# Optimization experiments

Hardware: AMD Instinct MI355X
Metric: run time of the kernel (lower is better)

Reference implementation:

```python
import jax, jax.numpy as jnp
import numpy as np

D_MODEL, N_HEADS, N_KV, THETA = 2048, 16, 4, 10000.0
HEAD_DIM = D_MODEL // N_HEADS  # 128


def _rope_sin_cos(seq_len, head_dim, theta):
    inv_freq = 1.0 / theta ** (jnp.arange(0, head_dim, 2, dtype=jnp.float32) / head_dim)
    pos = jnp.arange(seq_len, dtype=jnp.float32)
    freqs = pos[:, None] * inv_freq[None, :]              # [S, hd/2]
    emb = jnp.concatenate([freqs, freqs], axis=-1)        # [S, hd]
    return jnp.sin(emb), jnp.cos(emb)


def _rotate_half(t):
    h = t.shape[-1] // 2
    return jnp.concatenate([-t[..., h:], t[..., :h]], axis=-1)


def _apply_rope(t, sin, cos):
    # t: [B, H, S, hd]; sin/cos: [S, hd]
    return t * cos[None, None] + _rotate_half(t) * sin[None, None]


def setup_inputs() -> dict:
    key = jax.random.key(0)
    ks = jax.random.split(key, 5)
    B, S = 4, 2048
    scale = 1.0 / np.sqrt(D_MODEL)
    return {
        "x": jax.random.normal(ks[0], (B, S, D_MODEL), jnp.float32),
        "Wq": jax.random.normal(ks[1], (D_MODEL, N_HEADS * HEAD_DIM), jnp.float32) * scale,
        "Wk": jax.random.normal(ks[2], (D_MODEL, N_KV * HEAD_DIM), jnp.float32) * scale,
        "Wv": jax.random.normal(ks[3], (D_MODEL, N_KV * HEAD_DIM), jnp.float32) * scale,
        "Wo": jax.random.normal(ks[4], (N_HEADS * HEAD_DIM, D_MODEL), jnp.float32) * scale,
    }


def reference(x, Wq, Wk, Wv, Wo):
    B, S, _ = x.shape
    G = N_HEADS // N_KV  # query heads per kv head

    q = (x @ Wq).reshape(B, S, N_HEADS, HEAD_DIM).transpose(0, 2, 1, 3)  # [B,H,S,hd]
    k = (x @ Wk).reshape(B, S, N_KV, HEAD_DIM).transpose(0, 2, 1, 3)     # [B,KV,S,hd]
    v = (x @ Wv).reshape(B, S, N_KV, HEAD_DIM).transpose(0, 2, 1, 3)

    sin, cos = _rope_sin_cos(S, HEAD_DIM, THETA)
    q = _apply_rope(q, sin, cos)
    k = _apply_rope(k, sin, cos)

    # grouped attention: avoid materializing repeated kv heads
    qg = q.reshape(B, N_KV, G, S, HEAD_DIM)
    scores = jnp.einsum("bkgqd,bksd->bkgqs", qg, k) / np.sqrt(HEAD_DIM)
    causal = jnp.tril(jnp.ones((S, S), dtype=bool))
    scores = jnp.where(causal[None, None, None], scores, jnp.finfo(scores.dtype).min)
    attn = jax.nn.softmax(scores, axis=-1)
    out = jnp.einsum("bkgqs,bksd->bkgqd", attn, v)          # [B,KV,G,S,hd]
    out = out.reshape(B, N_HEADS, S, HEAD_DIM).transpose(0, 2, 1, 3).reshape(B, S, N_HEADS * HEAD_DIM)
    return out @ Wo
```

## Files before the change

kernel.cpp:

```cpp
#include <hip/hip_runtime.h>
#include <hip/hip_bf16.h>

#define DMODEL 2048
#define NHEADS 16
#define NKV 4
#define HD 128
#define SEQ 2048
#define BATCH 4

typedef __attribute__((ext_vector_type(2))) float f32x2;
typedef __attribute__((ext_vector_type(4))) float f32x4;
typedef __attribute__((ext_vector_type(16))) float f32x16;
typedef __attribute__((ext_vector_type(8))) short bf16x8;
typedef __attribute__((ext_vector_type(4))) unsigned int u32x4;

static __device__ __forceinline__ float bf2f(short u) {
    unsigned int x = ((unsigned int)(unsigned short)u) << 16;
    return __builtin_bit_cast(float, x);
}
static __device__ __forceinline__ short f2bf(float f) {
    unsigned int x = __builtin_bit_cast(unsigned int, f);
    unsigned int r = (x + 0x7fffu + ((x >> 16) & 1u)) >> 16;
    return (short)r;
}
static __device__ __forceinline__ unsigned int cvtpk_bf16(float lo, float hi) {
    unsigned int r;
    asm("v_cvt_pk_bf16_f32 %0, %1, %2" : "=v"(r) : "v"(lo), "v"(hi));
    return r;
}
static __device__ __forceinline__ float fexp2(float x) {
    float r;
    asm("v_exp_f32 %0, %1" : "=v"(r) : "v"(x));
    return r;
}
static __device__ __forceinline__ float ffract(float x) {
    float r;
    asm("v_fract_f32 %0, %1" : "=v"(r) : "v"(x));
    return r;
}
static __device__ __forceinline__ float fsin01(float x) {
    float r;
    asm("v_sin_f32 %0, %1" : "=v"(r) : "v"(x));
    return r;
}
static __device__ __forceinline__ float fcos01(float x) {
    float r;
    asm("v_cos_f32 %0, %1" : "=v"(r) : "v"(x));
    return r;
}
static __device__ __forceinline__ void gload16(const void* g, void* l) {
    __builtin_amdgcn_global_load_lds((const __attribute__((address_space(1))) void*)g,
                                     (__attribute__((address_space(3))) void*)l, 16, 0, 0);
}
static __device__ __forceinline__ void wbar6() {
    asm volatile("s_waitcnt vmcnt(6)" ::: "memory");
    __builtin_amdgcn_s_barrier();
    asm volatile("" ::: "memory");
}
static __device__ __forceinline__ void wbar4() {
    asm volatile("s_waitcnt vmcnt(4)" ::: "memory");
    __builtin_amdgcn_s_barrier();
    asm volatile("" ::: "memory");
}
static __device__ __forceinline__ void wbar6lg() {
    asm volatile("s_waitcnt vmcnt(6) lgkmcnt(0)" ::: "memory");
    __builtin_amdgcn_s_barrier();
    asm volatile("" ::: "memory");
}
static __device__ __forceinline__ void wbar0lg() {
    asm volatile("s_waitcnt vmcnt(0) lgkmcnt(0)" ::: "memory");
    __builtin_amdgcn_s_barrier();
    asm volatile("" ::: "memory");
}
static __device__ __forceinline__ void bar() {
    __builtin_amdgcn_s_barrier();
    asm volatile("" ::: "memory");
}

__global__ __launch_bounds__(256)
void prep(const float* __restrict__ x, short* __restrict__ xb,
          const float* __restrict__ Wq, const float* __restrict__ Wk,
          const float* __restrict__ Wv, const float* __restrict__ Wo,
          short* __restrict__ WqkvT, short* __restrict__ WoT) {
    __shared__ short Ts[64 * 72];
    const int bid = blockIdx.x, tid = threadIdx.x;

    if (bid < 2048) {
        const int n8 = BATCH * SEQ * DMODEL / 8;
        for (int i = bid * 256 + tid; i < n8; i += 2048 * 256) {
            float4 a = ((const float4*)x)[(size_t)i * 2];
            float4 b = ((const float4*)x)[(size_t)i * 2 + 1];
            bf16x8 o;
            o[0] = f2bf(a.x); o[1] = f2bf(a.y); o[2] = f2bf(a.z); o[3] = f2bf(a.w);
            o[4] = f2bf(b.x); o[5] = f2bf(b.y); o[6] = f2bf(b.z); o[7] = f2bf(b.w);
            ((bf16x8*)xb)[i] = o;
        }
        return;
    }

    const float* W;
    short* Wt;
    int C, r0, c0;
    if (bid < 3072) {
        int id = bid - 2048;
        W = Wq; Wt = WqkvT; C = 2048;
        c0 = (id & 31) * 64; r0 = (id >> 5) * 64;
    } else if (bid < 3328) {
        int id = bid - 3072;
        W = Wk; Wt = WqkvT + (size_t)2048 * 2048; C = 512;
        c0 = (id & 7) * 64; r0 = (id >> 3) * 64;
    } else if (bid < 3584) {
        int id = bid - 3328;
        W = Wv; Wt = WqkvT + (size_t)2560 * 2048; C = 512;
        c0 = (id & 7) * 64; r0 = (id >> 3) * 64;
    } else {
        int id = bid - 3584;
        W = Wo; Wt = WoT; C = 2048;
        c0 = (id & 31) * 64; r0 = (id >> 5) * 64;
    }
    const int R = 2048;
    for (int it = 0; it < 4; ++it) {
        int idx = it * 256 + tid;
        int row = idx >> 4, col4 = (idx & 15) * 4;
        float4 t = *(const float4*)&W[(size_t)(r0 + row) * C + c0 + col4];
        Ts[(col4 + 0) * 72 + row] = f2bf(t.x);
        Ts[(col4 + 1) * 72 + row] = f2bf(t.y);
        Ts[(col4 + 2) * 72 + row] = f2bf(t.z);
        Ts[(col4 + 3) * 72 + row] = f2bf(t.w);
    }
    __syncthreads();
    for (int it = 0; it < 2; ++it) {
        int idx = it * 256 + tid;
        int n = idx >> 3, k8 = (idx & 7) * 8;
        bf16x8 o = *(const bf16x8*)&Ts[n * 72 + k8];
        *(bf16x8*)&Wt[(size_t)(c0 + n) * R + r0 + k8] = o;
    }
}

template <int MODE>
__global__ __launch_bounds__(256, 2)
void gemm_sb(const short* __restrict__ A, const short* __restrict__ B,
             void* __restrict__ Cp, int M, int N, int K, int nbx) {
    __shared__ short As[256 * 64];
    __shared__ short Bs[128 * 64];
    const int tid = threadIdx.x, lane = tid & 63, w = tid >> 6;
    const int wr = w >> 1, wc = w & 1, lr = lane & 15, lg = lane >> 4;

    const int nwg = gridDim.x;
    const int qq = nwg >> 3, rr = nwg & 7;
    const int xcd = blockIdx.x & 7, loc = blockIdx.x >> 3;
    const int wg = (xcd < rr ? xcd * (qq + 1) : rr * (qq + 1) + (xcd - rr) * qq) + loc;
    const int m0 = (wg / nbx) * 256, n0 = (wg % nbx) * 128;

    const int srcchunk = ((lane & 7) ^ (lane >> 3)) * 8;
    const int lrow = w * 8;
    const int grow = w * 8 + (lane >> 3);

#define STG_A(T, HA)                                                              \
    {                                                                             \
        _Pragma("unroll") for (int i = 0; i < 4; ++i)                             \
            gload16(&A[(size_t)(m0 + (HA) * 128 + i * 32 + grow) * K +            \
                       (size_t)(T) * 64 + srcchunk],                              \
                    &As[((HA) * 128 + i * 32 + lrow) * 64]);                      \
    }
#define STG_B(T, HB)                                                              \
    {                                                                             \
        _Pragma("unroll") for (int i = 0; i < 2; ++i)                             \
            gload16(&B[(size_t)(n0 + (HB) * 64 + i * 32 + grow) * K +             \
                       (size_t)(T) * 64 + srcchunk],                              \
                    &Bs[((HB) * 64 + i * 32 + lrow) * 64]);                       \
    }

    f32x4 acc[2][4][2][2] = {};
    const int NT = K >> 6;

    STG_A(0, 0);
    STG_B(0, 0);
    STG_B(0, 1);
    STG_A(0, 1);

    bf16x8 af0[4][2], af1[4][2], bf0[2][2], bf1[2][2];
    for (int kt = 0; kt < NT; ++kt) {
        const int Tn = (kt + 1 < NT) ? kt + 1 : kt;

        wbar6();
#pragma unroll
        for (int q = 0; q < 4; ++q)
#pragma unroll
            for (int kk = 0; kk < 2; ++kk)
                af0[q][kk] = *(const bf16x8*)&As[(wr * 64 + q * 16 + lr) * 64 +
                                                 (((kk * 4 + lg) ^ (lr & 7)) << 3)];
#pragma unroll
        for (int r = 0; r < 2; ++r)
#pragma unroll
            for (int kk = 0; kk < 2; ++kk)
                bf0[r][kk] = *(const bf16x8*)&Bs[(wc * 32 + r * 16 + lr) * 64 +
                                                 (((kk * 4 + lg) ^ (lr & 7)) << 3)];
        __builtin_amdgcn_s_setprio(1);
#pragma unroll
        for (int q = 0; q < 4; ++q)
#pragma unroll
            for (int r = 0; r < 2; ++r)
#pragma unroll
                for (int kk = 0; kk < 2; ++kk)
                    acc[0][q][0][r] = __builtin_amdgcn_mfma_f32_16x16x32_bf16(
                        af0[q][kk], bf0[r][kk], acc[0][q][0][r], 0, 0, 0);
        __builtin_amdgcn_s_setprio(0);

        wbar4();
#pragma unroll
        for (int r = 0; r < 2; ++r)
#pragma unroll
            for (int kk = 0; kk < 2; ++kk)
                bf1[r][kk] = *(const bf16x8*)&Bs[(64 + wc * 32 + r * 16 + lr) * 64 +
                                                 (((kk * 4 + lg) ^ (lr & 7)) << 3)];
        STG_A(Tn, 0);
        STG_B(Tn, 0);
        __builtin_amdgcn_s_setprio(1);
#pragma unroll
        for (int q = 0; q < 4; ++q)
#pragma unroll
            for (int r = 0; r < 2; ++r)
#pragma unroll
                for (int kk = 0; kk < 2; ++kk)
                    acc[0][q][1][r] = __builtin_amdgcn_mfma_f32_16x16x32_bf16(
                        af0[q][kk], bf1[r][kk], acc[0][q][1][r], 0, 0, 0);
        __builtin_amdgcn_s_setprio(0);

        wbar6();
#pragma unroll
        for (int q = 0; q < 4; ++q)
#pragma unroll
            for (int kk = 0; kk < 2; ++kk)
                af1[q][kk] = *(const bf16x8*)&As[(128 + wr * 64 + q * 16 + lr) * 64 +
                                                 (((kk * 4 + lg) ^ (lr & 7)) << 3)];
        STG_B(Tn, 1);
        __builtin_amdgcn_s_setprio(1);
#pragma unroll
        for (int q = 0; q < 4; ++q)
#pragma unroll
            for (int r = 0; r < 2; ++r)
#pragma unroll
                for (int kk = 0; kk < 2; ++kk)
                    acc[1][q][0][r] = __builtin_amdgcn_mfma_f32_16x16x32_bf16(
                        af1[q][kk], bf0[r][kk], acc[1][q][0][r], 0, 0, 0);
        __builtin_amdgcn_s_setprio(0);

        bar();
        STG_A(Tn, 1);
        __builtin_amdgcn_s_setprio(1);
#pragma unroll
        for (int q = 0; q < 4; ++q)
#pragma unroll
            for (int r = 0; r < 2; ++r)
#pragma unroll
                for (int kk = 0; kk < 2; ++kk)
                    acc[1][q][1][r] = __builtin_amdgcn_mfma_f32_16x16x32_bf16(
                        af1[q][kk], bf1[r][kk], acc[1][q][1][r], 0, 0, 0);
        __builtin_amdgcn_s_setprio(0);
    }
    asm volatile("s_waitcnt vmcnt(0)" ::: "memory");

    if (MODE == 2 && n0 < 2560) {
        short* Cb = (short*)Cp;
        const float scl = (n0 >= 2048) ? 0.12751744695179782f : 1.0f;
        const float c13 = 13.287712379549449f / 64.0f;
        const float inv2pi = 0.15915494309189535f;
        float invf2[2];
#pragma unroll
        for (int r = 0; r < 2; ++r)
            invf2[r] = fexp2(-(float)(wc * 32 + r * 16 + lr) * c13) * inv2pi;
#pragma unroll
        for (int hA = 0; hA < 2; ++hA)
#pragma unroll
            for (int q = 0; q < 4; ++q)
#pragma unroll
                for (int r = 0; r < 2; ++r)
#pragma unroll
                    for (int j = 0; j < 4; ++j) {
                        int row = m0 + hA * 128 + wr * 64 + q * 16 + lg * 4 + j;
                        int pos = row & (SEQ - 1);
                        float fr = ffract((float)pos * invf2[r]);
                        float s = fsin01(fr), c = fcos01(fr);
                        float v0 = acc[hA][q][0][r][j];
                        float v1 = acc[hA][q][1][r][j];
                        int col0 = n0 + wc * 32 + r * 16 + lr;
                        Cb[(size_t)row * N + col0] = f2bf((v0 * c - v1 * s) * scl);
                        Cb[(size_t)row * N + col0 + 64] = f2bf((v1 * c + v0 * s) * scl);
                    }
    } else {
#pragma unroll
        for (int hA = 0; hA < 2; ++hA)
#pragma unroll
            for (int q = 0; q < 4; ++q)
#pragma unroll
                for (int hB = 0; hB < 2; ++hB)
#pragma unroll
                    for (int r = 0; r < 2; ++r)
#pragma unroll
                        for (int j = 0; j < 4; ++j) {
                            int row = m0 + hA * 128 + wr * 64 + q * 16 + lg * 4 + j;
                            int col = n0 + hB * 64 + wc * 32 + r * 16 + lr;
                            float v = acc[hA][q][hB][r][j];
                            if (MODE == 1) ((float*)Cp)[(size_t)row * N + col] = v;
                            else ((short*)Cp)[(size_t)row * N + col] = f2bf(v);
                        }
    }
#undef STG_A
#undef STG_B
}

template <bool A_F32, bool C_F32>
__global__ __launch_bounds__(256)
void gemm_kernel(const void* __restrict__ Ap, const float* __restrict__ Bp,
                 void* __restrict__ Cp, int M, int N, int K) {
    const int BK = 32, PAD = 8, LDT = BK + PAD;
    __shared__ short As[128 * LDT];
    __shared__ short Bt[128 * LDT];
    const int tid = threadIdx.x;
    const int lane = tid & 63, w = tid >> 6;
    const int wr = w >> 1, wc = w & 1;
    const int lr = lane & 15, lg = lane >> 4;
    const int m0 = blockIdx.y * 128, n0 = blockIdx.x * 128;
    f32x4 acc[4][4] = {};

    for (int k0 = 0; k0 < K; k0 += BK) {
        __syncthreads();
        for (int it = 0; it < 4; ++it) {
            int row = (tid >> 3) + it * 32;
            int kk = (tid & 7) * 4;
            short4 o;
            if (A_F32) {
                const float* A = (const float*)Ap;
                float4 t = *(const float4*)&A[(size_t)(m0 + row) * K + k0 + kk];
                o.x = f2bf(t.x); o.y = f2bf(t.y); o.z = f2bf(t.z); o.w = f2bf(t.w);
            } else {
                const short* A = (const short*)Ap;
                o = *(const short4*)&A[(size_t)(m0 + row) * K + k0 + kk];
            }
            *(short4*)&As[row * LDT + kk] = o;
        }
        for (int it = 0; it < 4; ++it) {
            int krow = (tid >> 5) + it * 8;
            int col = (tid & 31) * 4;
            float4 t = *(const float4*)&Bp[(size_t)(k0 + krow) * N + n0 + col];
            Bt[(col + 0) * LDT + krow] = f2bf(t.x);
            Bt[(col + 1) * LDT + krow] = f2bf(t.y);
            Bt[(col + 2) * LDT + krow] = f2bf(t.z);
            Bt[(col + 3) * LDT + krow] = f2bf(t.w);
        }
        __syncthreads();
        bf16x8 af[4], bfr[4];
        for (int rb = 0; rb < 4; ++rb)
            af[rb] = *(const bf16x8*)&As[(wr * 64 + rb * 16 + lr) * LDT + lg * 8];
        for (int cb = 0; cb < 4; ++cb)
            bfr[cb] = *(const bf16x8*)&Bt[(wc * 64 + cb * 16 + lr) * LDT + lg * 8];
        for (int rb = 0; rb < 4; ++rb)
            for (int cb = 0; cb < 4; ++cb)
                acc[rb][cb] = __builtin_amdgcn_mfma_f32_16x16x32_bf16(
                    af[rb], bfr[cb], acc[rb][cb], 0, 0, 0);
    }

    for (int rb = 0; rb < 4; ++rb)
        for (int cb = 0; cb < 4; ++cb)
            for (int j = 0; j < 4; ++j) {
                int row = m0 + wr * 64 + rb * 16 + lg * 4 + j;
                int col = n0 + wc * 64 + cb * 16 + lr;
                float v = acc[rb][cb][j];
                if (C_F32) ((float*)Cp)[(size_t)row * N + col] = v;
                else ((short*)Cp)[(size_t)row * N + col] = f2bf(v);
            }
}

__global__ __launch_bounds__(256)
void rope_kernel(short* __restrict__ Qp, int ldq, short* __restrict__ Kp, int ldk) {
    const int QP = BATCH * SEQ * NHEADS * 64;
    const int KP = BATCH * SEQ * NKV * 64;
    const int total = QP + KP;
    const float kscale = 0.12751744695179782f;
    for (int idx = blockIdx.x * blockDim.x + threadIdx.x; idx < total;
         idx += gridDim.x * blockDim.x) {
        short* base;
        size_t off;
        int i, row;
        float scl;
        if (idx < QP) {
            i = idx & 63;
            int hh = (idx >> 6) & (NHEADS - 1);
            row = idx >> 10;
            base = Qp;
            off = (size_t)row * ldq + hh * HD;
            scl = 1.0f;
        } else {
            int t = idx - QP;
            i = t & 63;
            int hh = (t >> 6) & (NKV - 1);
            row = t >> 8;
            base = Kp;
            off = (size_t)row * ldk + hh * HD;
            scl = kscale;
        }
        int pos = row & (SEQ - 1);
        float invf = exp2f(-(float)i * (13.287712379549449f / 64.0f));
        float ang = (float)pos * invf;
        float s, c;
        sincosf(ang, &s, &c);
        float t1 = bf2f(base[off + i]);
        float t2 = bf2f(base[off + i + 64]);
        base[off + i] = f2bf((t1 * c - t2 * s) * scl);
        base[off + i + 64] = f2bf((t2 * c + t1 * s) * scl);
    }
}

__global__ __launch_bounds__(512, 2)
void attn_kernel(const short* __restrict__ Qp, int ldq,
                 const short* __restrict__ Kp, int ldk,
                 const short* __restrict__ Vp, int ldv,
                 short* __restrict__ O) {
    __shared__ short Ks[3][64 * 128];
    __shared__ short Vt[2][128 * 64];

    const int tid = threadIdx.x, lane = tid & 63, w = tid >> 6;
    const int l31 = lane & 31, lh = lane >> 5, l7 = lane & 7;
    const int hq = blockIdx.y, b = blockIdx.z;
    const int kvh = hq >> 2;
    const size_t brow = (size_t)b * SEQ;

    const int d0 = (tid & 15) * 8;
    const int rvb = (tid >> 4) * 2;
    bf16x8 vreg[2];

#define STAGE_K(T, BUF)                                                              \
    {                                                                                \
        _Pragma("unroll") for (int it = 0; it < 2; ++it) {                           \
            int row = w * 8 + it * 4 + (lane >> 4);                                  \
            int cblk = (lane & 15) ^ (row & 7);                                      \
            gload16(&Kp[(brow + (size_t)(T) * 64 + row) * ldk + kvh * HD + cblk * 8],\
                    &Ks[BUF][(w * 8 + it * 4) * 128]);                               \
        }                                                                            \
    }
#define LOAD_V(T)                                                                    \
    {                                                                                \
        _Pragma("unroll") for (int h2 = 0; h2 < 2; ++h2)                             \
            vreg[h2] = *(const bf16x8*)&Vp[(brow + (size_t)(T) * 64 + rvb + h2) *    \
                                           ldv + kvh * HD + d0];                     \
    }
#define WRITE_V(BUF)                                                                 \
    {                                                                                \
        _Pragma("unroll") for (int e = 0; e < 8; ++e) {                              \
            int dd = d0 + e;                                                         \
            int gg = (e ^ (tid & 15)) & 7;                                           \
            unsigned int pk = ((unsigned int)(unsigned short)vreg[0][e]) |           \
                              (((unsigned int)(unsigned short)vreg[1][e]) << 16);    \
            *(unsigned int*)&Vt[BUF][dd * 64 + (((rvb >> 3) ^ gg) << 3) + (rvb & 7)] = pk;\
        }                                                                            \
    }

    for (int pass = 0; pass < 2; ++pass) {
        const int qt = (pass == 0) ? (int)blockIdx.x : 7 - (int)blockIdx.x;
        const int q0 = qt * 256;
        const int qrow = q0 + w * 32 + l31;

        bf16x8 qf[8];
#pragma unroll
        for (int kc = 0; kc < 8; ++kc)
            qf[kc] = *(const bf16x8*)&Qp[(brow + qrow) * ldq + hq * HD +
                                         kc * 16 + lh * 8];

        f32x16 oacc[4] = {};
        float mrun = -__builtin_inff(), lrun = 0.f;

        const int ntiles = 4 * qt + 4;

        __syncthreads();
        STAGE_K(0, 0);
        LOAD_V(0);
        __syncthreads();
        WRITE_V(0);
        STAGE_K(1, 1);
        LOAD_V(1);
        __syncthreads();

        int cur = 0;
        int kcur = 0;
        for (int t = 0; t < ntiles; ++t) {
            const int nxt = cur ^ 1;
            const bool pre = (t + 1 < ntiles);
            const bool deep = (t + 2 < ntiles);
            const int kb2 = (kcur >= 1) ? kcur - 1 : kcur + 2;

            if (deep) { STAGE_K(t + 2, kb2); }

            f32x16 sacc[2] = {};
            __builtin_amdgcn_s_setprio(1);
#pragma unroll
            for (int kvb = 0; kvb < 2; ++kvb) {
                const int kvrow = kvb * 32 + l31;
#pragma unroll
                for (int kc = 0; kc < 8; ++kc) {
                    int c = kc * 2 + lh;
                    int cp = (c & 8) | ((c ^ l7) & 7);
                    bf16x8 kf = *(const bf16x8*)&Ks[kcur][kvrow * 128 + cp * 8];
                    sacc[kvb] = __builtin_amdgcn_mfma_f32_32x32x16_bf16(
                        kf, qf[kc], sacc[kvb], 0, 0, 0);
                }
            }
            __builtin_amdgcn_s_setprio(0);

            const int kv0 = t * 64;
            float st[32];
            const bool need_mask = (kv0 + 63 > qrow);
#pragma unroll
            for (int kvb = 0; kvb < 2; ++kvb)
#pragma unroll
                for (int r = 0; r < 16; ++r) {
                    float s = sacc[kvb][r];
                    if (need_mask) {
                        int kvloc = kvb * 32 + (r & 3) + 8 * (r >> 2) + 4 * lh;
                        if (kv0 + kvloc > qrow) s = -__builtin_inff();
                    }
                    st[kvb * 16 + r] = s;
                }

            f32x2 p2[16];
#pragma unroll
            for (int i = 0; i < 16; ++i) p2[i] = (f32x2){st[2 * i], st[2 * i + 1]};

            f32x2 x8[8], x4[4], x2v[2], x1;
#pragma unroll
            for (int i = 0; i < 8; ++i) x8[i] = __builtin_elementwise_max(p2[i], p2[i + 8]);
#pragma unroll
            for (int i = 0; i < 4; ++i) x4[i] = __builtin_elementwise_max(x8[i], x8[i + 4]);
            x2v[0] = __builtin_elementwise_max(x4[0], x4[2]);
            x2v[1] = __builtin_elementwise_max(x4[1], x4[3]);
            x1 = __builtin_elementwise_max(x2v[0], x2v[1]);
            float rowmax = fmaxf(x1[0], x1[1]);
            rowmax = fmaxf(rowmax, __shfl_xor(rowmax, 32, 64));

            if (!__all(rowmax <= mrun + 11.54f)) {
                float mnew = fmaxf(mrun, rowmax);
                float alpha = fexp2(mrun - mnew);
                lrun *= alpha;
#pragma unroll
                for (int db = 0; db < 4; ++db)
#pragma unroll
                    for (int r = 0; r < 16; ++r) oacc[db][r] *= alpha;
                mrun = mnew;
            }
            const f32x2 mr2 = (f32x2){mrun, mrun};
#pragma unroll
            for (int i = 0; i < 16; ++i) {
                f32x2 d = p2[i] - mr2;
                st[2 * i] = fexp2(d[0]);
                st[2 * i + 1] = fexp2(d[1]);
            }
            f32x2 q2[16];
#pragma unroll
            for (int i = 0; i < 16; ++i) q2[i] = (f32x2){st[2 * i], st[2 * i + 1]};
            f32x2 t8[8], t4[4], t2v[2], t1;
#pragma unroll
            for (int i = 0; i < 8; ++i) t8[i] = q2[i] + q2[i + 8];
#pragma unroll
            for (int i = 0; i < 4; ++i) t4[i] = t8[i] + t8[i + 4];
            t2v[0] = t4[0] + t4[2];
            t2v[1] = t4[1] + t4[3];
            t1 = t2v[0] + t2v[1];
            float rs = t1[0] + t1[1];
            rs += __shfl_xor(rs, 32, 64);
            lrun += rs;

            if (pre) {
                WRITE_V(nxt);
                if (deep) { LOAD_V(t + 2); }
            }

            u32x4 pfrag[4];
#pragma unroll
            for (int kvc = 0; kvc < 4; ++kvc) {
                int base2 = (kvc >> 1) * 16 + (kvc & 1) * 8;
                unsigned int lo0 = cvtpk_bf16(st[base2 + 0], st[base2 + 1]);
                unsigned int lo1 = cvtpk_bf16(st[base2 + 2], st[base2 + 3]);
                unsigned int hi0 = cvtpk_bf16(st[base2 + 4], st[base2 + 5]);
                unsigned int hi1 = cvtpk_bf16(st[base2 + 6], st[base2 + 7]);
                unsigned int rlo0 = __shfl_xor(lo0, 32, 64);
                unsigned int rlo1 = __shfl_xor(lo1, 32, 64);
                unsigned int rhi0 = __shfl_xor(hi0, 32, 64);
                unsigned int rhi1 = __shfl_xor(hi1, 32, 64);
                u32x4 pu;
                pu[0] = lh ? rhi0 : lo0;
                pu[1] = lh ? rhi1 : lo1;
                pu[2] = lh ? hi0 : rlo0;
                pu[3] = lh ? hi1 : rlo1;
                pfrag[kvc] = pu;
            }

            __builtin_amdgcn_s_setprio(1);
#pragma unroll
            for (int db = 0; db < 4; ++db) {
                const int d = db * 32 + l31;
                const int g = (d ^ (d >> 3)) & 7;
#pragma unroll
                for (int kvc = 0; kvc < 4; ++kvc) {
                    int cp = ((kvc * 2 + lh) ^ g) & 7;
                    bf16x8 vf = *(const bf16x8*)&Vt[cur][d * 64 + cp * 8];
                    oacc[db] = __builtin_amdgcn_mfma_f32_32x32x16_bf16(
                        vf, __builtin_bit_cast(bf16x8, pfrag[kvc]), oacc[db], 0, 0, 0);
                }
            }
            __builtin_amdgcn_s_setprio(0);

            if (pre) {
                if (deep) { wbar6lg(); } else { wbar0lg(); }
                cur = nxt;
                kcur = (kcur < 2) ? kcur + 1 : 0;
            }
        }

        const float invl = 1.0f / lrun;
#pragma unroll
        for (int db = 0; db < 4; ++db)
#pragma unroll
            for (int j = 0; j < 4; ++j) {
                short4 o4;
                o4.x = f2bf(oacc[db][j * 4 + 0] * invl);
                o4.y = f2bf(oacc[db][j * 4 + 1] * invl);
                o4.z = f2bf(oacc[db][j * 4 + 2] * invl);
                o4.w = f2bf(oacc[db][j * 4 + 3] * invl);
                *(short4*)&O[(brow + qrow) * DMODEL + hq * HD +
                             db * 32 + 8 * j + 4 * lh] = o4;
            }
    }
#undef STAGE_K
#undef LOAD_V
#undef WRITE_V
}

extern "C" void kernel_launch(void* const* d_in, const int* in_sizes, int n_in,
                              void* d_out, int out_size, void* d_ws, size_t ws_size,
                              hipStream_t stream) {
    const float* x = (const float*)d_in[0];
    const float* Wq = (const float*)d_in[1];
    const float* Wk = (const float*)d_in[2];
    const float* Wv = (const float*)d_in[3];
    const float* Wo = (const float*)d_in[4];
    float* out = (float*)d_out;

    const size_t BS = (size_t)BATCH * SEQ;
    dim3 blk(256);

    const size_t planA_shorts = BS * 2048 + BS * 3072 + (size_t)3072 * 2048 + (size_t)2048 * 2048;
    if (ws_size >= planA_shorts * 2) {
        short* xb = (short*)d_ws;
        short* QKV = xb + BS * 2048;
        short* WqkvT = QKV + BS * 3072;
        short* WoT = WqkvT + (size_t)3072 * 2048;
        short* AO = xb;

        prep<<<dim3(4608), blk, 0, stream>>>(x, xb, Wq, Wk, Wv, Wo, WqkvT, WoT);
        gemm_sb<2><<<dim3(768), blk, 0, stream>>>(xb, WqkvT, (void*)QKV,
                                                  8192, 3072, 2048, 24);
        attn_kernel<<<dim3(4, NHEADS, BATCH), dim3(512), 0, stream>>>(
            QKV, 3072, QKV + 2048, 3072, QKV + 2560, 3072, AO);
        gemm_sb<1><<<dim3(512), blk, 0, stream>>>(AO, WoT, (void*)out,
                                                  8192, 2048, 2048, 16);
    } else {
        short* Qb = (short*)d_ws;
        short* Kb = Qb + BS * DMODEL;
        short* Vb = Kb + BS * (NKV * HD);
        short* AO = Vb + BS * (NKV * HD);
        gemm_kernel<true, false><<<dim3(16, 64), blk, 0, stream>>>((const void*)x, Wq, (void*)Qb, 8192, 2048, 2048);
        gemm_kernel<true, false><<<dim3(4, 64), blk, 0, stream>>>((const void*)x, Wk, (void*)Kb, 8192, 512, 2048);
        gemm_kernel<true, false><<<dim3(4, 64), blk, 0, stream>>>((const void*)x, Wv, (void*)Vb, 8192, 512, 2048);
        rope_kernel<<<dim3(4096), blk, 0, stream>>>(Qb, 2048, Kb, 512);
        attn_kernel<<<dim3(4, NHEADS, BATCH), dim3(512), 0, stream>>>(
            Qb, 2048, Kb, 512, Vb, 512, AO);
        gemm_kernel<false, true><<<dim3(16, 64), blk, 0, stream>>>((const void*)AO, Wo, (void*)out, 8192, 2048, 2048);
    }
}
```

Before: 322.0 us.

## Software-pipeline QK^T of next tile with softmax of current tile

The attention loop is unrolled by two with ping-pong score accumulators, so the QK^T MFMAs for tile t+1 are issued before the softmax and PV of tile t. The goal is to overlap matrix-core work with the exponent and reduction VALU work. The barrier wait count drops from vmcnt(6) to vmcnt(2), so the K tile staged two steps ahead is resident one iteration earlier. The extra 32 accumulator registers raise register pressure, and the tighter wait can expose more global-load latency.

New measurement: 408.3 us. 1.27x slower.

```diff
diff --git a/kernel.cpp b/kernel.cpp
--- a/kernel.cpp
+++ b/kernel.cpp
@@ -62,8 +62,8 @@
     __builtin_amdgcn_s_barrier();
     asm volatile("" ::: "memory");
 }
-static __device__ __forceinline__ void wbar6lg() {
-    asm volatile("s_waitcnt vmcnt(6) lgkmcnt(0)" ::: "memory");
+static __device__ __forceinline__ void wbar2lg() {
+    asm volatile("s_waitcnt vmcnt(2) lgkmcnt(0)" ::: "memory");
     __builtin_amdgcn_s_barrier();
     asm volatile("" ::: "memory");
 }
@@ -455,6 +455,123 @@
             *(unsigned int*)&Vt[BUF][dd * 64 + (((rvb >> 3) ^ gg) << 3) + (rvb & 7)] = pk;\
         }                                                                            \
     }
+#define QK_ISSUE(SDST, KBUF)                                                         \
+    {                                                                                \
+        SDST[0] = (f32x16){};                                                        \
+        SDST[1] = (f32x16){};                                                        \
+        __builtin_amdgcn_s_setprio(1);                                               \
+        _Pragma("unroll") for (int kvb = 0; kvb < 2; ++kvb) {                        \
+            const int kvrow = kvb * 32 + l31;                                        \
+            _Pragma("unroll") for (int kc = 0; kc < 8; ++kc) {                       \
+                int c = kc * 2 + lh;                                                 \
+                int cp = (c & 8) | ((c ^ l7) & 7);                                   \
+                bf16x8 kf = *(const bf16x8*)&Ks[KBUF][kvrow * 128 + cp * 8];         \
+                SDST[kvb] = __builtin_amdgcn_mfma_f32_32x32x16_bf16(                 \
+                    kf, qf[kc], SDST[kvb], 0, 0, 0);                                 \
+            }                                                                        \
+        }                                                                            \
+        __builtin_amdgcn_s_setprio(0);                                               \
+    }
+#define TILE_BODY(T, SCUR, SNEXT)                                                    \
+    {                                                                                \
+        const int nxt = cur ^ 1;                                                     \
+        const bool pre = ((T) + 1 < ntiles);                                         \
+        const bool deep = ((T) + 2 < ntiles);                                        \
+        const int kb2 = (kcur >= 1) ? kcur - 1 : kcur + 2;                           \
+        const int knx = (kcur < 2) ? kcur + 1 : 0;                                   \
+        if (deep) { STAGE_K((T) + 2, kb2); }                                         \
+        if (pre) { QK_ISSUE(SNEXT, knx); }                                           \
+        const int kv0 = (T) * 64;                                                    \
+        float st[32];                                                                \
+        const bool need_mask = (kv0 + 63 > qrow);                                    \
+        _Pragma("unroll") for (int kvb = 0; kvb < 2; ++kvb)                          \
+            _Pragma("unroll") for (int r = 0; r < 16; ++r) {                         \
+                float s = SCUR[kvb][r];                                              \
+                if (need_mask) {                                                     \
+                    int kvloc = kvb * 32 + (r & 3) + 8 * (r >> 2) + 4 * lh;          \
+                    if (kv0 + kvloc > qrow) s = -__builtin_inff();                   \
+                }                                                                    \
+                st[kvb * 16 + r] = s;                                                \
+            }                                                                        \
+        f32x2 p2[16];                                                                \
+        _Pragma("unroll") for (int i = 0; i < 16; ++i)                               \
+            p2[i] = (f32x2){st[2 * i], st[2 * i + 1]};                               \
+        f32x2 x8[8], x4[4], x2v[2], x1;                                              \
+        _Pragma("unroll") for (int i = 0; i < 8; ++i)                                \
+            x8[i] = __builtin_elementwise_max(p2[i], p2[i + 8]);                     \
+        _Pragma("unroll") for (int i = 0; i < 4; ++i)                                \
+            x4[i] = __builtin_elementwise_max(x8[i], x8[i + 4]);                     \
+        x2v[0] = __builtin_elementwise_max(x4[0], x4[2]);                            \
+        x2v[1] = __builtin_elementwise_max(x4[1], x4[3]);                            \
+        x1 = __builtin_elementwise_max(x2v[0], x2v[1]);                              \
+        float rowmax = fmaxf(x1[0], x1[1]);                                          \
+        rowmax = fmaxf(rowmax, __shfl_xor(rowmax, 32, 64));                          \
+        if (!__all(rowmax <= mrun + 11.54f)) {                                       \
+            float mnew = fmaxf(mrun, rowmax);                                        \
+            float alpha = fexp2(mrun - mnew);                                        \
+            lrun *= alpha;                                                           \
+            _Pragma("unroll") for (int db = 0; db < 4; ++db)                         \
+                _Pragma("unroll") for (int r = 0; r < 16; ++r) oacc[db][r] *= alpha; \
+            mrun = mnew;                                                             \
+        }                                                                            \
+        const f32x2 mr2 = (f32x2){mrun, mrun};                                       \
+        _Pragma("unroll") for (int i = 0; i < 16; ++i) {                             \
+            f32x2 dd2 = p2[i] - mr2;                                                 \
+            st[2 * i] = fexp2(dd2[0]);                                               \
+            st[2 * i + 1] = fexp2(dd2[1]);                                           \
+        }                                                                            \
+        f32x2 q2[16];                                                                \
+        _Pragma("unroll") for (int i = 0; i < 16; ++i)                               \
+            q2[i] = (f32x2){st[2 * i], st[2 * i + 1]};                               \
+        f32x2 t8[8], t4[4], t2v[2], t1;                                              \
+        _Pragma("unroll") for (int i = 0; i < 8; ++i) t8[i] = q2[i] + q2[i + 8];     \
+        _Pragma("unroll") for (int i = 0; i < 4; ++i) t4[i] = t8[i] + t8[i + 4];     \
+        t2v[0] = t4[0] + t4[2];                                                      \
+        t2v[1] = t4[1] + t4[3];                                                      \
+        t1 = t2v[0] + t2v[1];                                                        \
+        float rs = t1[0] + t1[1];                                                    \
+        rs += __shfl_xor(rs, 32, 64);                                                \
+        lrun += rs;                                                                  \
+        if (pre) {                                                                   \
+            WRITE_V(nxt);                                                            \
+            if (deep) { LOAD_V((T) + 2); }                                           \
+        }                                                                            \
+        u32x4 pfrag[4];                                                              \
+        _Pragma("unroll") for (int kvc = 0; kvc < 4; ++kvc) {                        \
+            int base2 = (kvc >> 1) * 16 + (kvc & 1) * 8;                             \
+            unsigned int lo0 = cvtpk_bf16(st[base2 + 0], st[base2 + 1]);             \
+            unsigned int lo1 = cvtpk_bf16(st[base2 + 2], st[base2 + 3]);             \
+            unsigned int hi0 = cvtpk_bf16(st[base2 + 4], st[base2 + 5]);             \
+            unsigned int hi1 = cvtpk_bf16(st[base2 + 6], st[base2 + 7]);             \
+            unsigned int rlo0 = __shfl_xor(lo0, 32, 64);                             \
+            unsigned int rlo1 = __shfl_xor(lo1, 32, 64);                             \
+            unsigned int rhi0 = __shfl_xor(hi0, 32, 64);                             \
+            unsigned int rhi1 = __shfl_xor(hi1, 32, 64);                             \
+            u32x4 pu;                                                                \
+            pu[0] = lh ? rhi0 : lo0;                                                 \
+            pu[1] = lh ? rhi1 : lo1;                                                 \
+            pu[2] = lh ? hi0 : rlo0;                                                 \
+            pu[3] = lh ? hi1 : rlo1;                                                 \
+            pfrag[kvc] = pu;                                                         \
+        }                                                                            \
+        __builtin_amdgcn_s_setprio(1);                                               \
+        _Pragma("unroll") for (int db = 0; db < 4; ++db) {                           \
+            const int d = db * 32 + l31;                                             \
+            const int g = (d ^ (d >> 3)) & 7;                                        \
+            _Pragma("unroll") for (int kvc = 0; kvc < 4; ++kvc) {                    \
+                int cp = ((kvc * 2 + lh) ^ g) & 7;                                   \
+                bf16x8 vf = *(const bf16x8*)&Vt[cur][d * 64 + cp * 8];               \
+                oacc[db] = __builtin_amdgcn_mfma_f32_32x32x16_bf16(                  \
+                    vf, __builtin_bit_cast(bf16x8, pfrag[kvc]), oacc[db], 0, 0, 0);  \
+            }                                                                        \
+        }                                                                            \
+        __builtin_amdgcn_s_setprio(0);                                               \
+        if (pre) {                                                                   \
+            if (deep) { wbar2lg(); } else { wbar0lg(); }                             \
+            cur = nxt;                                                               \
+            kcur = knx;                                                              \
+        }                                                                            \
+    }
 
     for (int pass = 0; pass < 2; ++pass) {
         const int qt = (pass == 0) ? (int)blockIdx.x : 7 - (int)blockIdx.x;
@@ -483,137 +600,12 @@
 
         int cur = 0;
         int kcur = 0;
-        for (int t = 0; t < ntiles; ++t) {
-            const int nxt = cur ^ 1;
-            const bool pre = (t + 1 < ntiles);
-            const bool deep = (t + 2 < ntiles);
-            const int kb2 = (kcur >= 1) ? kcur - 1 : kcur + 2;
-
-            if (deep) { STAGE_K(t + 2, kb2); }
-
-            f32x16 sacc[2] = {};
-            __builtin_amdgcn_s_setprio(1);
-#pragma unroll
-            for (int kvb = 0; kvb < 2; ++kvb) {
-                const int kvrow = kvb * 32 + l31;
-#pragma unroll
-                for (int kc = 0; kc < 8; ++kc) {
-                    int c = kc * 2 + lh;
-                    int cp = (c & 8) | ((c ^ l7) & 7);
-                    bf16x8 kf = *(const bf16x8*)&Ks[kcur][kvrow * 128 + cp * 8];
-                    sacc[kvb] = __builtin_amdgcn_mfma_f32_32x32x16_bf16(
-                        kf, qf[kc], sacc[kvb], 0, 0, 0);
-                }
-            }
-            __builtin_amdgcn_s_setprio(0);
-
-            const int kv0 = t * 64;
-            float st[32];
-            const bool need_mask = (kv0 + 63 > qrow);
-#pragma unroll
-            for (int kvb = 0; kvb < 2; ++kvb)
-#pragma unroll
-                for (int r = 0; r < 16; ++r) {
-                    float s = sacc[kvb][r];
-                    if (need_mask) {
-                        int kvloc = kvb * 32 + (r & 3) + 8 * (r >> 2) + 4 * lh;
-                        if (kv0 + kvloc > qrow) s = -__builtin_inff();
-                    }
-                    st[kvb * 16 + r] = s;
-                }
-
-            f32x2 p2[16];
-#pragma unroll
-            for (int i = 0; i < 16; ++i) p2[i] = (f32x2){st[2 * i], st[2 * i + 1]};
-
-            f32x2 x8[8], x4[4], x2v[2], x1;
-#pragma unroll
-            for (int i = 0; i < 8; ++i) x8[i] = __builtin_elementwise_max(p2[i], p2[i + 8]);
-#pragma unroll
-            for (int i = 0; i < 4; ++i) x4[i] = __builtin_elementwise_max(x8[i], x8[i + 4]);
-            x2v[0] = __builtin_elementwise_max(x4[0], x4[2]);
-            x2v[1] = __builtin_elementwise_max(x4[1], x4[3]);
-            x1 = __builtin_elementwise_max(x2v[0], x2v[1]);
-            float rowmax = fmaxf(x1[0], x1[1]);
-            rowmax = fmaxf(rowmax, __shfl_xor(rowmax, 32, 64));
-
-            if (!__all(rowmax <= mrun + 11.54f)) {
-                float mnew = fmaxf(mrun, rowmax);
-                float alpha = fexp2(mrun - mnew);
-                lrun *= alpha;
-#pragma unroll
-                for (int db = 0; db < 4; ++db)
-#pragma unroll
-                    for (int r = 0; r < 16; ++r) oacc[db][r] *= alpha;
-                mrun = mnew;
-            }
-            const f32x2 mr2 = (f32x2){mrun, mrun};
-#pragma unroll
-            for (int i = 0; i < 16; ++i) {
-                f32x2 d = p2[i] - mr2;
-                st[2 * i] = fexp2(d[0]);
-                st[2 * i + 1] = fexp2(d[1]);
-            }
-            f32x2 q2[16];
-#pragma unroll
-            for (int i = 0; i < 16; ++i) q2[i] = (f32x2){st[2 * i], st[2 * i + 1]};
-            f32x2 t8[8], t4[4], t2v[2], t1;
-#pragma unroll
-            for (int i = 0; i < 8; ++i) t8[i] = q2[i] + q2[i + 8];
-#pragma unroll
-            for (int i = 0; i < 4; ++i) t4[i] = t8[i] + t8[i + 4];
-            t2v[0] = t4[0] + t4[2];
-            t2v[1] = t4[1] + t4[3];
-            t1 = t2v[0] + t2v[1];
-            float rs = t1[0] + t1[1];
-            rs += __shfl_xor(rs, 32, 64);
-            lrun += rs;
-
-            if (pre) {
-                WRITE_V(nxt);
-                if (deep) { LOAD_V(t + 2); }
-            }
-
-            u32x4 pfrag[4];
-#pragma unroll
-            for (int kvc = 0; kvc < 4; ++kvc) {
-                int base2 = (kvc >> 1) * 16 + (kvc & 1) * 8;
-                unsigned int lo0 = cvtpk_bf16(st[base2 + 0], st[base2 + 1]);
-                unsigned int lo1 = cvtpk_bf16(st[base2 + 2], st[base2 + 3]);
-                unsigned int hi0 = cvtpk_bf16(st[base2 + 4], st[base2 + 5]);
-                unsigned int hi1 = cvtpk_bf16(st[base2 + 6], st[base2 + 7]);
-                unsigned int rlo0 = __shfl_xor(lo0, 32, 64);
-                unsigned int rlo1 = __shfl_xor(lo1, 32, 64);
-                unsigned int rhi0 = __shfl_xor(hi0, 32, 64);
-                unsigned int rhi1 = __shfl_xor(hi1, 32, 64);
-                u32x4 pu;
-                pu[0] = lh ? rhi0 : lo0;
-                pu[1] = lh ? rhi1 : lo1;
-                pu[2] = lh ? hi0 : rlo0;
-                pu[3] = lh ? hi1 : rlo1;
-                pfrag[kvc] = pu;
-            }
-
-            __builtin_amdgcn_s_setprio(1);
-#pragma unroll
-            for (int db = 0; db < 4; ++db) {
-                const int d = db * 32 + l31;
-                const int g = (d ^ (d >> 3)) & 7;
-#pragma unroll
-                for (int kvc = 0; kvc < 4; ++kvc) {
-                    int cp = ((kvc * 2 + lh) ^ g) & 7;
-                    bf16x8 vf = *(const bf16x8*)&Vt[cur][d * 64 + cp * 8];
-                    oacc[db] = __builtin_amdgcn_mfma_f32_32x32x16_bf16(
-                        vf, __builtin_bit_cast(bf16x8, pfrag[kvc]), oacc[db], 0, 0, 0);
-                }
-            }
-            __builtin_amdgcn_s_setprio(0);
-
-            if (pre) {
-                if (deep) { wbar6lg(); } else { wbar0lg(); }
-                cur = nxt;
-                kcur = (kcur < 2) ? kcur + 1 : 0;
-            }
+        f32x16 sA[2], sB[2];
+        QK_ISSUE(sA, 0);
+
+        for (int t = 0; t < ntiles; t += 2) {
+            TILE_BODY(t, sA, sB);
+            TILE_BODY(t + 1, sB, sA);
         }
 
         const float invl = 1.0f / lrun;
@@ -633,6 +625,8 @@
 #undef STAGE_K
 #undef LOAD_V
 #undef WRITE_V
+#undef QK_ISSUE
+#undef TILE_BODY
 }
 
 extern "C" void kernel_launch(void* const* d_in, const int* in_sizes, int n_in,
```

## Add 256x256-tile 8-wave pipelined GEMM for output projection

Applied to the files above, without the earlier changes.

Adds a new bf16 MFMA GEMM kernel with 256x256 tiles, 512 threads, double-buffered swizzled LDS, and interleaved staging of the next K tiles between MFMA quarter-steps with setprio. It also remaps block IDs across the 8 XCDs for locality. It replaces the 128-tile gemm_sb for the Wo projection, aiming for more data reuse per tile and better overlap of loads with compute. The trade-off is higher LDS and register use, which limits occupancy, and a grid of only 256 blocks.

After: 324.0 us. About the same (+0.6%).

```diff
diff --git a/kernel.cpp b/kernel.cpp
--- a/kernel.cpp
+++ b/kernel.cpp
@@ -308,6 +308,155 @@
     }
 #undef STG_A
 #undef STG_B
+}
+
+__global__ __launch_bounds__(512, 2)
+void gemm8(const short* __restrict__ A, const short* __restrict__ B,
+           float* __restrict__ C, int M, int N, int K, int nbx) {
+    __shared__ short As[2][256 * 64];
+    __shared__ short Bs[2][256 * 64];
+    const int tid = threadIdx.x, lane = tid & 63, w = tid >> 6;
+    const int wm = w >> 2, wn = w & 3;
+    const int lr = lane & 15, lg = lane >> 4;
+    const int l8 = lane >> 3, l7 = lane & 7;
+
+    const int nwg = gridDim.x;
+    const int qq = nwg >> 3, rr = nwg & 7;
+    const int xcd = blockIdx.x & 7, loc = blockIdx.x >> 3;
+    const int wg = (xcd < rr ? xcd * (qq + 1) : rr * (qq + 1) + (xcd - rr) * qq) + loc;
+    const int m0 = (wg / nbx) * 256, n0 = (wg % nbx) * 256;
+
+    const int srcchunk = (l7 ^ l8) * 8;
+    const int NT = K >> 6;
+
+#define STG_A8(T, MH, BUF)                                                         \
+    {                                                                              \
+        _Pragma("unroll") for (int j = 0; j < 2; ++j)                              \
+            gload16(&A[(size_t)(m0 + j * 128 + (MH) * 64 + w * 8 + l8) * K +       \
+                       (size_t)(T) * 64 + srcchunk],                               \
+                    &As[BUF][(j * 128 + (MH) * 64 + w * 8) * 64]);                 \
+    }
+#define STG_B8(T, NH, BUF)                                                         \
+    {                                                                              \
+        _Pragma("unroll") for (int j = 0; j < 2; ++j) {                            \
+            int rbase = (j * 2 + (w >> 2)) * 64 + (NH) * 32 + (w & 3) * 8;         \
+            gload16(&B[(size_t)(n0 + rbase + l8) * K +                             \
+                       (size_t)(T) * 64 + srcchunk],                               \
+                    &Bs[BUF][rbase * 64]);                                         \
+        }                                                                          \
+    }
+
+    f32x4 acc[2][4][2][2] = {};
+
+    STG_A8(0, 0, 0);
+    STG_A8(0, 1, 0);
+    STG_B8(0, 0, 0);
+    STG_B8(0, 1, 0);
+    STG_A8(1, 0, 1);
+    STG_B8(1, 0, 1);
+    wbar4();
+
+    bf16x8 af[4][2], b0[2][2], b1[2][2];
+    for (int t = 0; t < NT; ++t) {
+        const int bt = t & 1;
+        const int tn1 = (t + 1 < NT) ? t + 1 : NT - 1;
+        const int tn2 = (t + 2 < NT) ? t + 2 : NT - 1;
+        const int bn1 = tn1 & 1, bn2 = tn2 & 1;
+
+#pragma unroll
+        for (int mf = 0; mf < 4; ++mf)
+#pragma unroll
+            for (int kk = 0; kk < 2; ++kk)
+                af[mf][kk] = *(const bf16x8*)&As[bt][(wm * 128 + mf * 16 + lr) * 64 +
+                                                    (((kk * 4 + lg) ^ (lr & 7)) << 3)];
+#pragma unroll
+        for (int nf = 0; nf < 2; ++nf)
+#pragma unroll
+            for (int kk = 0; kk < 2; ++kk)
+                b0[nf][kk] = *(const bf16x8*)&Bs[bt][(wn * 64 + nf * 16 + lr) * 64 +
+                                                     (((kk * 4 + lg) ^ (lr & 7)) << 3)];
+        STG_A8(tn1, 1, bn1);
+        __builtin_amdgcn_s_setprio(1);
+#pragma unroll
+        for (int mf = 0; mf < 4; ++mf)
+#pragma unroll
+            for (int nf = 0; nf < 2; ++nf)
+#pragma unroll
+                for (int kk = 0; kk < 2; ++kk)
+                    acc[0][mf][0][nf] = __builtin_amdgcn_mfma_f32_16x16x32_bf16(
+                        af[mf][kk], b0[nf][kk], acc[0][mf][0][nf], 0, 0, 0);
+        __builtin_amdgcn_s_setprio(0);
+        bar();
+
+#pragma unroll
+        for (int nf = 0; nf < 2; ++nf)
+#pragma unroll
+            for (int kk = 0; kk < 2; ++kk)
+                b1[nf][kk] = *(const bf16x8*)&Bs[bt][(wn * 64 + 32 + nf * 16 + lr) * 64 +
+                                                     (((kk * 4 + lg) ^ (lr & 7)) << 3)];
+        STG_B8(tn1, 1, bn1);
+        __builtin_amdgcn_s_setprio(1);
+#pragma unroll
+        for (int mf = 0; mf < 4; ++mf)
+#pragma unroll
+            for (int nf = 0; nf < 2; ++nf)
+#pragma unroll
+                for (int kk = 0; kk < 2; ++kk)
+                    acc[0][mf][1][nf] = __builtin_amdgcn_mfma_f32_16x16x32_bf16(
+                        af[mf][kk], b1[nf][kk], acc[0][mf][1][nf], 0, 0, 0);
+        __builtin_amdgcn_s_setprio(0);
+        bar();
+
+#pragma unroll
+        for (int mf = 0; mf < 4; ++mf)
+#pragma unroll
+            for (int kk = 0; kk < 2; ++kk)
+                af[mf][kk] = *(const bf16x8*)&As[bt][(wm * 128 + 64 + mf * 16 + lr) * 64 +
+                                                    (((kk * 4 + lg) ^ (lr & 7)) << 3)];
+        STG_A8(tn2, 0, bn2);
+        __builtin_amdgcn_s_setprio(1);
+#pragma unroll
+        for (int mf = 0; mf < 4; ++mf)
+#pragma unroll
+            for (int nf = 0; nf < 2; ++nf)
+#pragma unroll
+                for (int kk = 0; kk < 2; ++kk)
+                    acc[1][mf][0][nf] = __builtin_amdgcn_mfma_f32_16x16x32_bf16(
+                        af[mf][kk], b0[nf][kk], acc[1][mf][0][nf], 0, 0, 0);
+        __builtin_amdgcn_s_setprio(0);
+        bar();
+
+        STG_B8(tn2, 0, bn2);
+        __builtin_amdgcn_s_setprio(1);
+#pragma unroll
+        for (int mf = 0; mf < 4; ++mf)
+#pragma unroll
+            for (int nf = 0; nf < 2; ++nf)
+#pragma unroll
+                for (int kk = 0; kk < 2; ++kk)
+                    acc[1][mf][1][nf] = __builtin_amdgcn_mfma_f32_16x16x32_bf16(
+                        af[mf][kk], b1[nf][kk], acc[1][mf][1][nf], 0, 0, 0);
+        __builtin_amdgcn_s_setprio(0);
+        wbar4();
+    }
+    asm volatile("s_waitcnt vmcnt(0)" ::: "memory");
+
+#pragma unroll
+    for (int mh = 0; mh < 2; ++mh)
+#pragma unroll
+        for (int mf = 0; mf < 4; ++mf)
+#pragma unroll
+            for (int nh = 0; nh < 2; ++nh)
+#pragma unroll
+                for (int nf = 0; nf < 2; ++nf)
+#pragma unroll
+                    for (int j = 0; j < 4; ++j) {
+                        int row = m0 + wm * 128 + mh * 64 + mf * 16 + lg * 4 + j;
+                        int col = n0 + wn * 64 + nh * 32 + nf * 16 + lr;
+                        C[(size_t)row * N + col] = acc[mh][mf][nh][nf][j];
+                    }
+#undef STG_A8
+#undef STG_B8
 }
 
 template <bool A_F32, bool C_F32>
@@ -661,8 +810,8 @@
                                                   8192, 3072, 2048, 24);
         attn_kernel<<<dim3(4, NHEADS, BATCH), dim3(512), 0, stream>>>(
             QKV, 3072, QKV + 2048, 3072, QKV + 2560, 3072, AO);
-        gemm_sb<1><<<dim3(512), blk, 0, stream>>>(AO, WoT, (void*)out,
-                                                  8192, 2048, 2048, 16);
+        gemm8<<<dim3(256), dim3(512), 0, stream>>>(AO, WoT, out,
+                                                   8192, 2048, 2048, 8);
     } else {
         short* Qb = (short*)d_ws;
         short* Kb = Qb + BS * DMODEL;
```
